# Kernel tuning notes

Hardware: AMD Instinct MI355X
Metric: run time of the kernel (lower is better)

Reference implementation:

```python
import jax, jax.numpy as jnp
import numpy as np


def setup_inputs() -> dict:
    key = jax.random.key(0)
    k1, k2, k3, k4 = jax.random.split(key, 4)
    d_in, d_out, B, T = 1024, 1024, 4, 2048
    scale = 1.0 / np.sqrt(d_in)
    return {
        "x": jax.random.normal(k1, (B, T, d_in), dtype=jnp.float32),
        "Wq": jax.random.normal(k2, (d_in, d_out), dtype=jnp.float32) * scale,
        "Wk": jax.random.normal(k3, (d_in, d_out), dtype=jnp.float32) * scale,
        "Wv": jax.random.normal(k4, (d_in, d_out), dtype=jnp.float32) * scale,
    }


def reference(x, Wq, Wk, Wv):
    # x: [B, T, d_in]; Wq/Wk/Wv: [d_in, d_out] (Linear, bias=False)
    q = jnp.einsum("btd,de->bte", x, Wq)
    k = jnp.einsum("btd,de->bte", x, Wk)
    v = jnp.einsum("btd,de->bte", x, Wv)
    d_out = k.shape[-1]
    scores = jnp.einsum("bqe,bke->bqk", q, k)  # [B, T, T]
    T = x.shape[1]
    causal = jnp.triu(jnp.ones((T, T), dtype=bool), k=1)  # True above diagonal
    scores = jnp.where(causal[None, :, :], -jnp.inf, scores)
    # original divides after masking; -inf stays -inf so math is identical
    att = jax.nn.softmax(scores / jnp.sqrt(jnp.asarray(d_out, scores.dtype)), axis=-1)
    # dropout p=0.0 -> identity
    return jnp.einsum("bqk,bke->bqe", att, v)
```

## Files before the change

kernel.cpp:

```cpp
#include <hip/hip_runtime.h>
#include <stdint.h>
#include <math.h>

typedef unsigned short u16;
typedef __bf16 bf16x8 __attribute__((ext_vector_type(8)));
typedef float f32x4 __attribute__((ext_vector_type(4)));

#define BK 64

enum { M_QKV = 0, M_SCORE = 1, M_PV = 2 };

__device__ __forceinline__ u16 f2bf(float f) {
    union { float f; unsigned int u; } a; a.f = f;
    unsigned int u = a.u;
    u += 0x7FFFu + ((u >> 16) & 1u);
    return (u16)(u >> 16);
}

__device__ __forceinline__ void async_load16(const void* g, void* l) {
    __builtin_amdgcn_global_load_lds(
        (const __attribute__((address_space(1))) void*)g,
        (__attribute__((address_space(3))) void*)l,
        16, 0, 0);
}

template<int MODE>
__global__ __launch_bounds__(256)
void gemm_bt(const u16* __restrict__ A, long long sAb,
             const u16* __restrict__ Bt, long long sBb,
             void* __restrict__ Cv, long long sCb,
             float* __restrict__ rowsum,
             int M, int N, int K, float kfac)
{
    int bm, bn;
    if (MODE == M_SCORE) {
        const int idx = blockIdx.x;
        bm = (int)((sqrtf(8.f * idx + 1.f) - 1.f) * 0.5f);
        while ((bm + 1) * (bm + 2) / 2 <= idx) ++bm;
        while (bm * (bm + 1) / 2 > idx) --bm;
        bn = idx - bm * (bm + 1) / 2;
    } else {
        bn = blockIdx.x; bm = blockIdx.y;
    }
    const int bz = blockIdx.z;
    A  += (size_t)bz * sAb;
    Bt += (size_t)bz * sBb;

    const int tid  = threadIdx.x;
    const int lane = tid & 63;
    const int wv   = tid >> 6;
    const int wm   = wv >> 1;
    const int wn   = wv & 1;

    __shared__ __attribute__((aligned(16))) u16 As[128 * BK];
    __shared__ __attribute__((aligned(16))) u16 Bs[128 * BK];

    f32x4 acc[4][4] = {};

    const int rowA0 = bm * 128, rowB0 = bn * 128;
    const int srow = lane >> 3;
    const int scol = ((lane & 7) ^ (lane >> 3)) * 8;

    int kEnd = K;
    if (MODE == M_PV) { int ke = (bm + 1) * 128; kEnd = ke < K ? ke : K; }

    const int lm   = lane & 15;
    const int quad = lane >> 4;
    const int rx   = lm & 7;

    for (int k0 = 0; k0 < kEnd; k0 += BK) {
        #pragma unroll
        for (int c = 0; c < 4; ++c) {
            const int cc = wv * 4 + c;
            const int r  = cc * 8 + srow;
            async_load16(&A[(size_t)(rowA0 + r) * K + k0 + scol], &As[cc * 512 + lane * 8]);
        }
        #pragma unroll
        for (int c = 0; c < 4; ++c) {
            const int cc = wv * 4 + c;
            const int r  = cc * 8 + srow;
            async_load16(&Bt[(size_t)(rowB0 + r) * K + k0 + scol], &Bs[cc * 512 + lane * 8]);
        }
        __syncthreads();

        #pragma unroll
        for (int h = 0; h < 2; ++h) {
            const int slotb = h * 4 + quad;
            bf16x8 af[4], bfr[4];
            #pragma unroll
            for (int i = 0; i < 4; ++i)
                af[i] = *reinterpret_cast<const bf16x8*>(
                    &As[(wm * 64 + i * 16 + lm) * BK + (slotb ^ rx) * 8]);
            #pragma unroll
            for (int j = 0; j < 4; ++j)
                bfr[j] = *reinterpret_cast<const bf16x8*>(
                    &Bs[(wn * 64 + j * 16 + lm) * BK + (slotb ^ rx) * 8]);
            #pragma unroll
            for (int i = 0; i < 4; ++i)
                #pragma unroll
                for (int j = 0; j < 4; ++j)
                    acc[i][j] = __builtin_amdgcn_mfma_f32_16x16x32_bf16(af[i], bfr[j], acc[i][j], 0, 0, 0);
        }
        __syncthreads();
    }

    if (MODE == M_QKV) {
        u16* C = (u16*)Cv + (size_t)(bn >> 3) * sCb;
        #pragma unroll
        for (int i = 0; i < 4; ++i)
            #pragma unroll
            for (int j = 0; j < 4; ++j) {
                const int r0 = rowA0 + wm * 64 + i * 16 + quad * 4;
                const int c0 = (rowB0 + wn * 64 + j * 16 + lm) & 1023;
                #pragma unroll
                for (int g = 0; g < 4; ++g)
                    C[(size_t)(r0 + g) * 1024 + c0] = f2bf(acc[i][j][g]);
            }
    } else if (MODE == M_SCORE) {
        u16* E = (u16*)Cv + (size_t)bz * sCb;
        float rs[4][4];
        #pragma unroll
        for (int i = 0; i < 4; ++i)
            #pragma unroll
            for (int g = 0; g < 4; ++g) rs[i][g] = 0.f;
        #pragma unroll
        for (int i = 0; i < 4; ++i)
            #pragma unroll
            for (int j = 0; j < 4; ++j) {
                const int r0 = rowA0 + wm * 64 + i * 16 + quad * 4;
                const int c  = rowB0 + wn * 64 + j * 16 + lm;
                #pragma unroll
                for (int g = 0; g < 4; ++g) {
                    const int r = r0 + g;
                    float e = (c <= r) ? exp2f(acc[i][j][g] * kfac) : 0.f;
                    E[(size_t)r * N + c] = f2bf(e);
                    rs[i][g] += e;
                }
            }
        #pragma unroll
        for (int i = 0; i < 4; ++i)
            #pragma unroll
            for (int g = 0; g < 4; ++g) {
                float v = rs[i][g];
                v += __shfl_xor(v, 1); v += __shfl_xor(v, 2);
                v += __shfl_xor(v, 4); v += __shfl_xor(v, 8);
                rs[i][g] = v;
            }
        if (lm == 0) {
            #pragma unroll
            for (int i = 0; i < 4; ++i)
                #pragma unroll
                for (int g = 0; g < 4; ++g) {
                    const int r = rowA0 + wm * 64 + i * 16 + quad * 4 + g;
                    atomicAdd(&rowsum[(size_t)bz * M + r], rs[i][g]);
                }
        }
    } else {
        float* C = (float*)Cv + (size_t)bz * sCb;
        #pragma unroll
        for (int i = 0; i < 4; ++i) {
            const int r0 = rowA0 + wm * 64 + i * 16 + quad * 4;
            float inv[4];
            #pragma unroll
            for (int g = 0; g < 4; ++g)
                inv[g] = 1.f / rowsum[(size_t)bz * M + r0 + g];
            #pragma unroll
            for (int j = 0; j < 4; ++j) {
                const int c0 = rowB0 + wn * 64 + j * 16 + lm;
                #pragma unroll
                for (int g = 0; g < 4; ++g)
                    C[(size_t)(r0 + g) * N + c0] = acc[i][j][g] * inv[g];
            }
        }
    }
}

__global__ __launch_bounds__(256)
void cast_x(const float* __restrict__ x, u16* __restrict__ o, long long n)
{
    long long i = ((long long)blockIdx.x * blockDim.x + threadIdx.x) * 8;
    if (i >= n) return;
    const float4 a = *(const float4*)(x + i);
    const float4 b = *(const float4*)(x + i + 4);
    union { u16 u[8]; float4 v; } r;
    r.u[0] = f2bf(a.x); r.u[1] = f2bf(a.y); r.u[2] = f2bf(a.z); r.u[3] = f2bf(a.w);
    r.u[4] = f2bf(b.x); r.u[5] = f2bf(b.y); r.u[6] = f2bf(b.z); r.u[7] = f2bf(b.w);
    *(float4*)(o + i) = r.v;
}

__global__ __launch_bounds__(256)
void castT_w3(const float* __restrict__ W0, const float* __restrict__ W1,
              const float* __restrict__ W2, u16* __restrict__ Wt, int D)
{
    const float* W = blockIdx.z == 0 ? W0 : (blockIdx.z == 1 ? W1 : W2);
    u16* dst = Wt + (size_t)blockIdx.z * D * D;
    __shared__ u16 t[32][33];
    const int c0 = blockIdx.x * 32, r0 = blockIdx.y * 32;
    const int tx = threadIdx.x & 31, ty = threadIdx.x >> 5;
    #pragma unroll
    for (int s = 0; s < 32; s += 8)
        t[ty + s][tx] = f2bf(W[(size_t)(r0 + ty + s) * D + c0 + tx]);
    __syncthreads();
    #pragma unroll
    for (int s = 0; s < 32; s += 8)
        dst[(size_t)(c0 + ty + s) * D + r0 + tx] = t[tx][ty + s];
}

__global__ __launch_bounds__(256)
void transpose_b(const u16* __restrict__ V, long long sVb,
                 u16* __restrict__ Vt, long long sVtb, int rows, int cols)
{
    V  += (size_t)blockIdx.z * sVb;
    Vt += (size_t)blockIdx.z * sVtb;
    __shared__ u16 t[32][33];
    const int c0 = blockIdx.x * 32, r0 = blockIdx.y * 32;
    const int tx = threadIdx.x & 31, ty = threadIdx.x >> 5;
    #pragma unroll
    for (int s = 0; s < 32; s += 8)
        t[ty + s][tx] = V[(size_t)(r0 + ty + s) * cols + c0 + tx];
    __syncthreads();
    #pragma unroll
    for (int s = 0; s < 32; s += 8)
        Vt[(size_t)(c0 + ty + s) * rows + r0 + tx] = t[tx][ty + s];
}

extern "C" void kernel_launch(void* const* d_in, const int* in_sizes, int n_in,
                              void* d_out, int out_size, void* d_ws, size_t ws_size,
                              hipStream_t stream)
{
    const int B = 4, T = 2048, D = 1024;
    const float* x  = (const float*)d_in[0];
    const float* Wq = (const float*)d_in[1];
    const float* Wk = (const float*)d_in[2];
    const float* Wv = (const float*)d_in[3];
    float* out = (float*)d_out;

    const size_t nX = (size_t)B * T * D;
    u16* Xb = (u16*)d_ws;
    u16* Wt = Xb + nX;
    u16* Q  = Wt + 3 * (size_t)D * D;
    u16* Kb = Q + nX;
    u16* Vb = Kb + nX;
    u16* Vt = Vb + nX;
    char* rest = (char*)(Vt + nX);
    const size_t fixed   = (size_t)((char*)rest - (char*)d_ws);
    const size_t perb_E  = (size_t)T * T * 2;
    const size_t perb_rs = (size_t)T * 4;
    const bool full = ws_size >= fixed + (size_t)B * (perb_E + perb_rs);
    const int nb = full ? B : 1;
    u16*   E  = (u16*)rest;
    float* RS = (float*)(E + nb * (size_t)T * T);

    const float kfac = 1.4426950408889634f / 32.0f;
    const int nTri = (T / 128) * (T / 128 + 1) / 2;

    cast_x<<<dim3((unsigned)(nX / (8 * 256))), 256, 0, stream>>>(x, Xb, (long long)nX);
    castT_w3<<<dim3(D / 32, D / 32, 3), 256, 0, stream>>>(Wq, Wk, Wv, Wt, D);

    gemm_bt<M_QKV><<<dim3(3 * D / 128, (B * T) / 128, 1), 256, 0, stream>>>(
        Xb, 0, Wt, 0, Q, (long long)nX, nullptr, B * T, 3 * D, D, 0.f);

    if (full) {
        hipMemsetAsync(RS, 0, (size_t)B * T * 4, stream);
        gemm_bt<M_SCORE><<<dim3(nTri, 1, B), 256, 0, stream>>>(
            Q, (long long)T * D, Kb, (long long)T * D, E, (long long)T * T, RS,
            T, T, D, kfac);
        transpose_b<<<dim3(D / 32, T / 32, B), 256, 0, stream>>>(
            Vb, (long long)T * D, Vt, (long long)D * T, T, D);
        gemm_bt<M_PV><<<dim3(D / 128, T / 128, B), 256, 0, stream>>>(
            E, (long long)T * T, Vt, (long long)D * T, out, (long long)T * D, RS,
            T, D, T, 0.f);
    } else {
        for (int b = 0; b < B; ++b) {
            const size_t ob = (size_t)b * T * D;
            hipMemsetAsync(RS, 0, (size_t)T * 4, stream);
            gemm_bt<M_SCORE><<<dim3(nTri, 1, 1), 256, 0, stream>>>(
                Q + ob, 0, Kb + ob, 0, E, 0, RS, T, T, D, kfac);
            transpose_b<<<dim3(D / 32, T / 32, 1), 256, 0, stream>>>(
                Vb + ob, 0, Vt, 0, T, D);
            gemm_bt<M_PV><<<dim3(D / 128, T / 128, 1), 256, 0, stream>>>(
                E, 0, Vt, 0, out + ob, 0, RS, T, D, T, 0.f);
        }
    }
}
```

Baseline: 248.5 us.

## Use 64-row M tiles for causal score and PV GEMMs to trim masked work

Templates the GEMM on the M tile height and runs the score and PV kernels with 64-row tiles over 128-column tiles, using a new triangular index mapping (272 tiles). Finer M granularity skips more of the fully masked upper-triangle work in both QK^T and PV, and improves load balance across the causal shape. The cost is lower per-block arithmetic intensity (fewer MFMAs per B-tile load) and more blocks and atomics. The rowsum memset is also hoisted ahead of the GEMMs.

```diff
diff --git a/kernel.cpp b/kernel.cpp
--- a/kernel.cpp
+++ b/kernel.cpp
@@ -5,8 +5,6 @@
 typedef unsigned short u16;
 typedef __bf16 bf16x8 __attribute__((ext_vector_type(8)));
 typedef float f32x4 __attribute__((ext_vector_type(4)));
-
-#define BK 64
 
 enum { M_QKV = 0, M_SCORE = 1, M_PV = 2 };
 
@@ -24,7 +22,7 @@
         16, 0, 0);
 }
 
-template<int MODE>
+template<int MODE, int TBM>
 __global__ __launch_bounds__(256)
 void gemm_bt(const u16* __restrict__ A, long long sAb,
              const u16* __restrict__ Bt, long long sBb,
@@ -32,13 +30,19 @@
              float* __restrict__ rowsum,
              int M, int N, int K, float kfac)
 {
+    constexpr int KB  = 64;
+    constexpr int NI  = TBM / 32;
+    constexpr int ACH = TBM / 32;
+    constexpr int BCH = 4;
+
     int bm, bn;
     if (MODE == M_SCORE) {
         const int idx = blockIdx.x;
-        bm = (int)((sqrtf(8.f * idx + 1.f) - 1.f) * 0.5f);
-        while ((bm + 1) * (bm + 2) / 2 <= idx) ++bm;
-        while (bm * (bm + 1) / 2 > idx) --bm;
-        bn = idx - bm * (bm + 1) / 2;
+        int w = (int)sqrtf((float)idx + 0.5f);
+        while (w * w > idx) --w;
+        while ((w + 1) * (w + 1) <= idx) ++w;
+        if (idx < w * w + w) { bm = 2 * w - 1; bn = idx - w * w; }
+        else                 { bm = 2 * w;     bn = idx - (w * w + w); }
     } else {
         bn = blockIdx.x; bm = blockIdx.y;
     }
@@ -52,51 +56,52 @@
     const int wm   = wv >> 1;
     const int wn   = wv & 1;
 
-    __shared__ __attribute__((aligned(16))) u16 As[128 * BK];
-    __shared__ __attribute__((aligned(16))) u16 Bs[128 * BK];
-
-    f32x4 acc[4][4] = {};
-
-    const int rowA0 = bm * 128, rowB0 = bn * 128;
-    const int srow = lane >> 3;
-    const int scol = ((lane & 7) ^ (lane >> 3)) * 8;
+    __shared__ __attribute__((aligned(16))) u16 As[TBM * KB];
+    __shared__ __attribute__((aligned(16))) u16 Bs[128 * KB];
+
+    f32x4 acc[NI][4] = {};
+
+    const int rowA0 = bm * TBM, rowB0 = bn * 128;
+    const int lrow  = lane >> 3;
+    const int lslot = lane & 7;
+    const int sg    = (lslot ^ lrow) * 8;
 
     int kEnd = K;
-    if (MODE == M_PV) { int ke = (bm + 1) * 128; kEnd = ke < K ? ke : K; }
+    if (MODE == M_PV) { int ke = (bm + 1) * TBM; kEnd = ke < K ? ke : K; }
 
     const int lm   = lane & 15;
     const int quad = lane >> 4;
     const int rx   = lm & 7;
 
-    for (int k0 = 0; k0 < kEnd; k0 += BK) {
-        #pragma unroll
-        for (int c = 0; c < 4; ++c) {
-            const int cc = wv * 4 + c;
-            const int r  = cc * 8 + srow;
-            async_load16(&A[(size_t)(rowA0 + r) * K + k0 + scol], &As[cc * 512 + lane * 8]);
-        }
-        #pragma unroll
-        for (int c = 0; c < 4; ++c) {
-            const int cc = wv * 4 + c;
-            const int r  = cc * 8 + srow;
-            async_load16(&Bt[(size_t)(rowB0 + r) * K + k0 + scol], &Bs[cc * 512 + lane * 8]);
+    for (int k0 = 0; k0 < kEnd; k0 += KB) {
+        #pragma unroll
+        for (int c = 0; c < ACH; ++c) {
+            const int cc  = wv * ACH + c;
+            const int row = cc * 8 + lrow;
+            async_load16(&A[(size_t)(rowA0 + row) * K + k0 + sg], &As[cc * 512 + lane * 8]);
+        }
+        #pragma unroll
+        for (int c = 0; c < BCH; ++c) {
+            const int cc  = wv * BCH + c;
+            const int row = cc * 8 + lrow;
+            async_load16(&Bt[(size_t)(rowB0 + row) * K + k0 + sg], &Bs[cc * 512 + lane * 8]);
         }
         __syncthreads();
 
         #pragma unroll
         for (int h = 0; h < 2; ++h) {
-            const int slotb = h * 4 + quad;
-            bf16x8 af[4], bfr[4];
-            #pragma unroll
-            for (int i = 0; i < 4; ++i)
+            const int sl = (((h * 4 + quad) ^ rx) * 8);
+            bf16x8 af[NI], bfr[4];
+            #pragma unroll
+            for (int i = 0; i < NI; ++i)
                 af[i] = *reinterpret_cast<const bf16x8*>(
-                    &As[(wm * 64 + i * 16 + lm) * BK + (slotb ^ rx) * 8]);
+                    &As[(wm * (TBM / 2) + i * 16 + lm) * KB + sl]);
             #pragma unroll
             for (int j = 0; j < 4; ++j)
                 bfr[j] = *reinterpret_cast<const bf16x8*>(
-                    &Bs[(wn * 64 + j * 16 + lm) * BK + (slotb ^ rx) * 8]);
-            #pragma unroll
-            for (int i = 0; i < 4; ++i)
+                    &Bs[(wn * 64 + j * 16 + lm) * KB + sl]);
+            #pragma unroll
+            for (int i = 0; i < NI; ++i)
                 #pragma unroll
                 for (int j = 0; j < 4; ++j)
                     acc[i][j] = __builtin_amdgcn_mfma_f32_16x16x32_bf16(af[i], bfr[j], acc[i][j], 0, 0, 0);
@@ -107,10 +112,10 @@
     if (MODE == M_QKV) {
         u16* C = (u16*)Cv + (size_t)(bn >> 3) * sCb;
         #pragma unroll
-        for (int i = 0; i < 4; ++i)
+        for (int i = 0; i < NI; ++i)
             #pragma unroll
             for (int j = 0; j < 4; ++j) {
-                const int r0 = rowA0 + wm * 64 + i * 16 + quad * 4;
+                const int r0 = rowA0 + wm * (TBM / 2) + i * 16 + quad * 4;
                 const int c0 = (rowB0 + wn * 64 + j * 16 + lm) & 1023;
                 #pragma unroll
                 for (int g = 0; g < 4; ++g)
@@ -118,16 +123,16 @@
             }
     } else if (MODE == M_SCORE) {
         u16* E = (u16*)Cv + (size_t)bz * sCb;
-        float rs[4][4];
-        #pragma unroll
-        for (int i = 0; i < 4; ++i)
+        float rs[NI][4];
+        #pragma unroll
+        for (int i = 0; i < NI; ++i)
             #pragma unroll
             for (int g = 0; g < 4; ++g) rs[i][g] = 0.f;
         #pragma unroll
-        for (int i = 0; i < 4; ++i)
+        for (int i = 0; i < NI; ++i)
             #pragma unroll
             for (int j = 0; j < 4; ++j) {
-                const int r0 = rowA0 + wm * 64 + i * 16 + quad * 4;
+                const int r0 = rowA0 + wm * (TBM / 2) + i * 16 + quad * 4;
                 const int c  = rowB0 + wn * 64 + j * 16 + lm;
                 #pragma unroll
                 for (int g = 0; g < 4; ++g) {
@@ -138,7 +143,7 @@
                 }
             }
         #pragma unroll
-        for (int i = 0; i < 4; ++i)
+        for (int i = 0; i < NI; ++i)
             #pragma unroll
             for (int g = 0; g < 4; ++g) {
                 float v = rs[i][g];
@@ -148,18 +153,18 @@
             }
         if (lm == 0) {
             #pragma unroll
-            for (int i = 0; i < 4; ++i)
+            for (int i = 0; i < NI; ++i)
                 #pragma unroll
                 for (int g = 0; g < 4; ++g) {
-                    const int r = rowA0 + wm * 64 + i * 16 + quad * 4 + g;
+                    const int r = rowA0 + wm * (TBM / 2) + i * 16 + quad * 4 + g;
                     atomicAdd(&rowsum[(size_t)bz * M + r], rs[i][g]);
                 }
         }
     } else {
         float* C = (float*)Cv + (size_t)bz * sCb;
         #pragma unroll
-        for (int i = 0; i < 4; ++i) {
-            const int r0 = rowA0 + wm * 64 + i * 16 + quad * 4;
+        for (int i = 0; i < NI; ++i) {
+            const int r0 = rowA0 + wm * (TBM / 2) + i * 16 + quad * 4;
             float inv[4];
             #pragma unroll
             for (int g = 0; g < 4; ++g)
@@ -252,33 +257,34 @@
     float* RS = (float*)(E + nb * (size_t)T * T);
 
     const float kfac = 1.4426950408889634f / 32.0f;
-    const int nTri = (T / 128) * (T / 128 + 1) / 2;
+    const int nTri64 = 272;
+
+    hipMemsetAsync(RS, 0, (size_t)nb * T * 4, stream);
 
     cast_x<<<dim3((unsigned)(nX / (8 * 256))), 256, 0, stream>>>(x, Xb, (long long)nX);
     castT_w3<<<dim3(D / 32, D / 32, 3), 256, 0, stream>>>(Wq, Wk, Wv, Wt, D);
 
-    gemm_bt<M_QKV><<<dim3(3 * D / 128, (B * T) / 128, 1), 256, 0, stream>>>(
+    gemm_bt<M_QKV, 128><<<dim3(3 * D / 128, (B * T) / 128, 1), 256, 0, stream>>>(
         Xb, 0, Wt, 0, Q, (long long)nX, nullptr, B * T, 3 * D, D, 0.f);
 
     if (full) {
-        hipMemsetAsync(RS, 0, (size_t)B * T * 4, stream);
-        gemm_bt<M_SCORE><<<dim3(nTri, 1, B), 256, 0, stream>>>(
+        gemm_bt<M_SCORE, 64><<<dim3(nTri64, 1, B), 256, 0, stream>>>(
             Q, (long long)T * D, Kb, (long long)T * D, E, (long long)T * T, RS,
             T, T, D, kfac);
         transpose_b<<<dim3(D / 32, T / 32, B), 256, 0, stream>>>(
             Vb, (long long)T * D, Vt, (long long)D * T, T, D);
-        gemm_bt<M_PV><<<dim3(D / 128, T / 128, B), 256, 0, stream>>>(
+        gemm_bt<M_PV, 64><<<dim3(D / 128, T / 64, B), 256, 0, stream>>>(
             E, (long long)T * T, Vt, (long long)D * T, out, (long long)T * D, RS,
             T, D, T, 0.f);
     } else {
         for (int b = 0; b < B; ++b) {
             const size_t ob = (size_t)b * T * D;
-            hipMemsetAsync(RS, 0, (size_t)T * 4, stream);
-            gemm_bt<M_SCORE><<<dim3(nTri, 1, 1), 256, 0, stream>>>(
+            if (b) hipMemsetAsync(RS, 0, (size_t)T * 4, stream);
+            gemm_bt<M_SCORE, 64><<<dim3(nTri64, 1, 1), 256, 0, stream>>>(
                 Q + ob, 0, Kb + ob, 0, E, 0, RS, T, T, D, kfac);
             transpose_b<<<dim3(D / 32, T / 32, 1), 256, 0, stream>>>(
                 Vb + ob, 0, Vt, 0, T, D);
-            gemm_bt<M_PV><<<dim3(D / 128, T / 128, 1), 256, 0, stream>>>(
+            gemm_bt<M_PV, 64><<<dim3(D / 128, T / 64, 1), 256, 0, stream>>>(
                 E, 0, Vt, 0, out + ob, 0, RS, T, D, T, 0.f);
         }
     }
```

Result: no change. 247.4 us (-0.5%).
